# Kernel optimization log

Measured on AMD Instinct MI355X. Metric: run time of the kernel, lower is better.

The kernel has to match this reference:

```python
import jax, jax.numpy as jnp
import numpy as np

NEG = -1000000000.0

def setup_inputs() -> dict:
    key = jax.random.key(0)
    k1, k2, k3, k4 = jax.random.split(key, 4)
    B, T, D, V = 64, 512, 768, 20
    embeddings = jax.random.normal(k1, (B, T, D), dtype=jnp.float32)
    embeddings_mask = jax.random.randint(k2, (B, T), 0, 2, dtype=jnp.int32)
    value_mask = jax.random.randint(k3, (B, V), 0, 2, dtype=jnp.int32)
    value_weight = jax.random.normal(k4, (V, D), dtype=jnp.float32)
    return {"embeddings": embeddings, "embeddings_mask": embeddings_mask,
            "value_mask": value_mask, "value_weight": value_weight}

def reference(embeddings, embeddings_mask, value_mask, value_weight):
    # value attention: scores[b,t,v] = <emb[b,t], W[v]>  (torch does bcast-mul-sum)
    emb_mask = embeddings_mask.astype(jnp.float32)          # (B,T)
    scores = jnp.einsum('btd,vd->btv', embeddings, value_weight)
    scores = scores * emb_mask[:, :, None]                   # mask tokens
    value_scores = scores.sum(axis=1)                        # (B,V)
    value_scores = value_scores + (1.0 - value_mask.astype(jnp.float32)) * NEG
    value_probs = jax.nn.softmax(value_scores, axis=-1)      # (B,V)
    value_embedding = jnp.einsum('bv,vd->bd', value_probs, value_weight)
    # attention pooling over tokens using value_embedding as query
    pooling_scores = jnp.einsum('btd,bd->bt', embeddings, value_embedding)
    pooling_scores = pooling_scores + (1.0 - emb_mask) * NEG
    pooling_probs = jax.nn.softmax(pooling_scores, axis=-1)  # (B,T)
    pooled_embedding = jnp.einsum('btd,bt->bd', embeddings, pooling_probs)
    return (value_embedding, pooled_embedding, value_probs, pooling_probs)
```

## Files before the change

### kernel.cpp

```cpp
#include <hip/hip_runtime.h>
#include <math.h>

#define B 64
#define T 512
#define D 768
#define D4 192
#define V 20
#define NEG -1000000000.0f
#define TCH 32
#define NCH 16
#define NBLK (B * NCH)

__global__ __launch_bounds__(256) void k_sum_vdots(
    const float4* __restrict__ emb4, const int* __restrict__ emask,
    const float* __restrict__ W, float* __restrict__ pd) {
  const int bc = blockIdx.x, b = bc >> 4, c = bc & 15;
  const int tid = threadIdx.x, wave = tid >> 6, lane = tid & 63;
  __shared__ int sm[TCH];
  __shared__ int idx[TCH];
  __shared__ int scnt;
  __shared__ float4 lacc4[4][D4];
  __shared__ float msum[D];

  if (tid < TCH) sm[tid] = emask[b * T + c * TCH + tid];
  __syncthreads();
  if (tid == 0) {
    int n = 0;
    for (int t = 0; t < TCH; ++t)
      if (sm[t]) idx[n++] = t;
    scnt = n;
  }
  __syncthreads();
  const int cnt = scnt;
  const float4* eb = emb4 + ((size_t)b * T + (size_t)c * TCH) * D4;

  float4 s0 = {0.f, 0.f, 0.f, 0.f}, s1 = s0, s2 = s0;
  int i = wave;
  for (; i + 4 < cnt; i += 8) {
    const float4* ea = eb + (size_t)idx[i] * D4 + lane;
    const float4* ec = eb + (size_t)idx[i + 4] * D4 + lane;
    float4 a0 = ea[0], a1 = ea[64], a2 = ea[128];
    float4 b0 = ec[0], b1 = ec[64], b2 = ec[128];
    s0.x += a0.x + b0.x; s0.y += a0.y + b0.y;
    s0.z += a0.z + b0.z; s0.w += a0.w + b0.w;
    s1.x += a1.x + b1.x; s1.y += a1.y + b1.y;
    s1.z += a1.z + b1.z; s1.w += a1.w + b1.w;
    s2.x += a2.x + b2.x; s2.y += a2.y + b2.y;
    s2.z += a2.z + b2.z; s2.w += a2.w + b2.w;
  }
  if (i < cnt) {
    const float4* ea = eb + (size_t)idx[i] * D4 + lane;
    float4 a0 = ea[0], a1 = ea[64], a2 = ea[128];
    s0.x += a0.x; s0.y += a0.y; s0.z += a0.z; s0.w += a0.w;
    s1.x += a1.x; s1.y += a1.y; s1.z += a1.z; s1.w += a1.w;
    s2.x += a2.x; s2.y += a2.y; s2.z += a2.z; s2.w += a2.w;
  }
  lacc4[wave][lane] = s0;
  lacc4[wave][lane + 64] = s1;
  lacc4[wave][lane + 128] = s2;
  __syncthreads();
  if (tid < D4) {
    float4 a = lacc4[0][tid], x = lacc4[1][tid], y = lacc4[2][tid],
           z = lacc4[3][tid];
    float4 r;
    r.x = a.x + x.x + y.x + z.x;
    r.y = a.y + x.y + y.y + z.y;
    r.z = a.z + x.z + y.z + z.z;
    r.w = a.w + x.w + y.w + z.w;
    *(float4*)&msum[4 * tid] = r;
  }
  __syncthreads();
  for (int v = wave; v < V; v += 4) {
    float p = 0.f;
    const float* wv = W + (size_t)v * D;
    for (int j = 0; j < 12; ++j) {
      int d = lane + 64 * j;
      p += msum[d] * wv[d];
    }
    for (int off = 32; off; off >>= 1) p += __shfl_xor(p, off, 64);
    if (lane == 0) pd[bc * V + v] = p;
  }
}

__global__ __launch_bounds__(256) void k_fused_pool(
    const float4* __restrict__ emb4, const int* __restrict__ emask,
    const int* __restrict__ vmask, const float* __restrict__ W,
    const float* __restrict__ pd, float* __restrict__ vemb_out,
    float* __restrict__ vprobs_out, float* __restrict__ scores,
    float* __restrict__ pm, float* __restrict__ pl,
    float4* __restrict__ pacc4) {
  const int bc = blockIdx.x, b = bc >> 4, c = bc & 15;
  const int tid = threadIdx.x, wave = tid >> 6, lane = tid & 63;
  __shared__ int sm[TCH];
  __shared__ int idx[TCH];
  __shared__ int scnt;
  __shared__ float4 lacc4[4][D4];
  __shared__ float vemb[D];
  __shared__ float sc[V], pr[V];
  __shared__ float lm[4], ll[4], co4[4];

  if (tid < TCH) sm[tid] = emask[b * T + c * TCH + tid];
  __syncthreads();
  if (tid == 0) {
    int n = 0;
    for (int t = 0; t < TCH; ++t)
      if (sm[t]) idx[n++] = t;
    scnt = n;
  }

  if (tid < V) {
    float s = 0.f;
    for (int cc = 0; cc < NCH; ++cc) s += pd[(b * NCH + cc) * V + tid];
    sc[tid] = s + (vmask[b * V + tid] ? 0.f : NEG);
  }
  __syncthreads();
  if (tid == 0) {
    float m = sc[0];
    for (int v = 1; v < V; ++v) m = fmaxf(m, sc[v]);
    float ssum = 0.f;
    for (int v = 0; v < V; ++v) {
      float e = expf(sc[v] - m);
      pr[v] = e;
      ssum += e;
    }
    float inv = 1.f / ssum;
    for (int v = 0; v < V; ++v) {
      pr[v] *= inv;
      if (c == 0) vprobs_out[b * V + v] = pr[v];
    }
  }
  __syncthreads();
  for (int k = 0; k < 3; ++k) {
    int d = tid + 256 * k;
    float a = 0.f;
    for (int v = 0; v < V; ++v) a += pr[v] * W[(size_t)v * D + d];
    vemb[d] = a;
    if (c == 0) vemb_out[(size_t)b * D + d] = a;
  }
  __syncthreads();

  const int cnt = scnt;
  const float4* eb = emb4 + ((size_t)b * T + (size_t)c * TCH) * D4;
  const float4* vb = (const float4*)vemb;
  float4 ve0 = vb[lane], ve1 = vb[lane + 64], ve2 = vb[lane + 128];
  float* srow = scores + b * T + c * TCH;
  float m = NEG, l = 0.f;
  float4 a0 = {0.f, 0.f, 0.f, 0.f}, a1 = a0, a2 = a0;
  int i = wave;
  for (; i + 4 < cnt; i += 8) {
    int t0 = idx[i], t1 = idx[i + 4];
    const float4* ea = eb + (size_t)t0 * D4 + lane;
    const float4* ec = eb + (size_t)t1 * D4 + lane;
    float4 e0 = ea[0], e1 = ea[64], e2 = ea[128];
    float4 f0 = ec[0], f1 = ec[64], f2 = ec[128];
    float p0 = e0.x * ve0.x + e0.y * ve0.y + e0.z * ve0.z + e0.w * ve0.w +
               e1.x * ve1.x + e1.y * ve1.y + e1.z * ve1.z + e1.w * ve1.w +
               e2.x * ve2.x + e2.y * ve2.y + e2.z * ve2.z + e2.w * ve2.w;
    float p1 = f0.x * ve0.x + f0.y * ve0.y + f0.z * ve0.z + f0.w * ve0.w +
               f1.x * ve1.x + f1.y * ve1.y + f1.z * ve1.z + f1.w * ve1.w +
               f2.x * ve2.x + f2.y * ve2.y + f2.z * ve2.z + f2.w * ve2.w;
    for (int off = 32; off; off >>= 1) {
      p0 += __shfl_xor(p0, off, 64);
      p1 += __shfl_xor(p1, off, 64);
    }
    if (lane == 0) { srow[t0] = p0; srow[t1] = p1; }
    float mn = fmaxf(m, fmaxf(p0, p1));
    float scale = expf(m - mn);
    float w0 = expf(p0 - mn), w1 = expf(p1 - mn);
    l = l * scale + w0 + w1;
    a0.x = a0.x * scale + w0 * e0.x + w1 * f0.x;
    a0.y = a0.y * scale + w0 * e0.y + w1 * f0.y;
    a0.z = a0.z * scale + w0 * e0.z + w1 * f0.z;
    a0.w = a0.w * scale + w0 * e0.w + w1 * f0.w;
    a1.x = a1.x * scale + w0 * e1.x + w1 * f1.x;
    a1.y = a1.y * scale + w0 * e1.y + w1 * f1.y;
    a1.z = a1.z * scale + w0 * e1.z + w1 * f1.z;
    a1.w = a1.w * scale + w0 * e1.w + w1 * f1.w;
    a2.x = a2.x * scale + w0 * e2.x + w1 * f2.x;
    a2.y = a2.y * scale + w0 * e2.y + w1 * f2.y;
    a2.z = a2.z * scale + w0 * e2.z + w1 * f2.z;
    a2.w = a2.w * scale + w0 * e2.w + w1 * f2.w;
    m = mn;
  }
  if (i < cnt) {
    int t0 = idx[i];
    const float4* ea = eb + (size_t)t0 * D4 + lane;
    float4 e0 = ea[0], e1 = ea[64], e2 = ea[128];
    float p0 = e0.x * ve0.x + e0.y * ve0.y + e0.z * ve0.z + e0.w * ve0.w +
               e1.x * ve1.x + e1.y * ve1.y + e1.z * ve1.z + e1.w * ve1.w +
               e2.x * ve2.x + e2.y * ve2.y + e2.z * ve2.z + e2.w * ve2.w;
    for (int off = 32; off; off >>= 1) p0 += __shfl_xor(p0, off, 64);
    if (lane == 0) srow[t0] = p0;
    float mn = fmaxf(m, p0);
    float scale = expf(m - mn);
    float w0 = expf(p0 - mn);
    l = l * scale + w0;
    a0.x = a0.x * scale + w0 * e0.x; a0.y = a0.y * scale + w0 * e0.y;
    a0.z = a0.z * scale + w0 * e0.z; a0.w = a0.w * scale + w0 * e0.w;
    a1.x = a1.x * scale + w0 * e1.x; a1.y = a1.y * scale + w0 * e1.y;
    a1.z = a1.z * scale + w0 * e1.z; a1.w = a1.w * scale + w0 * e1.w;
    a2.x = a2.x * scale + w0 * e2.x; a2.y = a2.y * scale + w0 * e2.y;
    a2.z = a2.z * scale + w0 * e2.z; a2.w = a2.w * scale + w0 * e2.w;
    m = mn;
  }
  if (lane == 0) { lm[wave] = m; ll[wave] = l; }
  lacc4[wave][lane] = a0;
  lacc4[wave][lane + 64] = a1;
  lacc4[wave][lane + 128] = a2;
  __syncthreads();
  if (tid == 0) {
    float M = fmaxf(fmaxf(lm[0], lm[1]), fmaxf(lm[2], lm[3]));
    float L = 0.f;
    for (int w2 = 0; w2 < 4; ++w2) {
      float cw = expf(lm[w2] - M);
      co4[w2] = cw;
      L += ll[w2] * cw;
    }
    pm[bc] = M;
    pl[bc] = L;
  }
  __syncthreads();
  if (tid < D4) {
    float4 r = {0.f, 0.f, 0.f, 0.f};
    for (int w2 = 0; w2 < 4; ++w2) {
      float cw = co4[w2];
      float4 a = lacc4[w2][tid];
      r.x += cw * a.x; r.y += cw * a.y;
      r.z += cw * a.z; r.w += cw * a.w;
    }
    pacc4[(size_t)bc * D4 + tid] = r;
  }
}

__global__ __launch_bounds__(256) void k_finalize(
    const float* __restrict__ pm, const float* __restrict__ pl,
    const float4* __restrict__ pacc4, const float* __restrict__ scores,
    const int* __restrict__ emask, float* __restrict__ pooled,
    float* __restrict__ pprobs) {
  const int b = blockIdx.x, tid = threadIdx.x;
  __shared__ float co[NCH];
  __shared__ float sM, sinvL;
  if (tid == 0) {
    float M = NEG;
    for (int cc = 0; cc < NCH; ++cc) M = fmaxf(M, pm[b * NCH + cc]);
    float L = 0.f;
    for (int cc = 0; cc < NCH; ++cc)
      L += pl[b * NCH + cc] * expf(pm[b * NCH + cc] - M);
    float invL = 1.f / L;
    for (int cc = 0; cc < NCH; ++cc)
      co[cc] = expf(pm[b * NCH + cc] - M) * invL;
    sM = M;
    sinvL = invL;
  }
  __syncthreads();
  if (tid < D4) {
    float4 r = {0.f, 0.f, 0.f, 0.f};
    for (int cc = 0; cc < NCH; ++cc) {
      float cw = co[cc];
      float4 a = pacc4[(size_t)(b * NCH + cc) * D4 + tid];
      r.x += cw * a.x; r.y += cw * a.y;
      r.z += cw * a.z; r.w += cw * a.w;
    }
    ((float4*)pooled)[(size_t)b * D4 + tid] = r;
  }
  float M = sM, invL = sinvL;
  for (int k = 0; k < 2; ++k) {
    int t = tid + 256 * k;
    pprobs[b * T + t] =
        emask[b * T + t] ? expf(scores[b * T + t] - M) * invL : 0.f;
  }
}

extern "C" void kernel_launch(void* const* d_in, const int* in_sizes, int n_in,
                              void* d_out, int out_size, void* d_ws,
                              size_t ws_size, hipStream_t stream) {
  const float4* emb4 = (const float4*)d_in[0];
  const int* emask = (const int*)d_in[1];
  const int* vmask = (const int*)d_in[2];
  const float* W = (const float*)d_in[3];

  float* out = (float*)d_out;
  float* vemb_out = out;
  float* pooled_out = out + B * D;
  float* vprobs_out = out + 2 * B * D;
  float* pprobs_out = out + 2 * B * D + B * V;

  float* ws = (float*)d_ws;
  float* pacc = ws;
  float* scores = pacc + NBLK * D;
  float* pm = scores + B * T;
  float* pl = pm + NBLK;
  float* pd = pl + NBLK;

  k_sum_vdots<<<dim3(NBLK), dim3(256), 0, stream>>>(emb4, emask, W, pd);
  k_fused_pool<<<dim3(NBLK), dim3(256), 0, stream>>>(
      emb4, emask, vmask, W, pd, vemb_out, vprobs_out, scores, pm, pl,
      (float4*)pacc);
  k_finalize<<<dim3(B), dim3(256), 0, stream>>>(pm, pl, (const float4*)pacc,
                                                scores, emask, pooled_out,
                                                pprobs_out);
}
```

Before: 165.6 us.

## Unroll token loops to four rows, ballot-compact mask, use fast exp

The token-gather loops in both streaming kernels now load four masked rows per iteration instead of two, putting more independent global loads in flight per wave. The serial single-thread mask compaction is replaced by a wave ballot plus popcount prefix. expf is swapped for __expf throughout, and launch bounds now request occupancy of 4 blocks. These add register pressure and slightly lower exp accuracy, and the tail loops now step by four rows.

```diff
diff --git a/kernel.cpp b/kernel.cpp
--- a/kernel.cpp
+++ b/kernel.cpp
@@ -11,46 +11,61 @@
 #define NCH 16
 #define NBLK (B * NCH)
 
-__global__ __launch_bounds__(256) void k_sum_vdots(
+__device__ __forceinline__ void compact_idx(const int* sm, int* idx,
+                                            int* scnt, int tid) {
+  if (tid < 64) {
+    unsigned long long bal = __ballot(tid < TCH && sm[tid]);
+    if (tid < TCH && sm[tid]) {
+      int pos = __popcll(bal & ((1ull << tid) - 1ull));
+      idx[pos] = tid;
+    }
+    if (tid == 0) *scnt = (int)__popcll(bal);
+  }
+}
+
+__global__ __launch_bounds__(256, 4) void k_sum_vdots(
     const float4* __restrict__ emb4, const int* __restrict__ emask,
     const float* __restrict__ W, float* __restrict__ pd) {
   const int bc = blockIdx.x, b = bc >> 4, c = bc & 15;
   const int tid = threadIdx.x, wave = tid >> 6, lane = tid & 63;
-  __shared__ int sm[TCH];
-  __shared__ int idx[TCH];
-  __shared__ int scnt;
+  __shared__ int sm[TCH], idx[TCH], scnt;
   __shared__ float4 lacc4[4][D4];
   __shared__ float msum[D];
 
   if (tid < TCH) sm[tid] = emask[b * T + c * TCH + tid];
   __syncthreads();
-  if (tid == 0) {
-    int n = 0;
-    for (int t = 0; t < TCH; ++t)
-      if (sm[t]) idx[n++] = t;
-    scnt = n;
-  }
+  compact_idx(sm, idx, &scnt, tid);
   __syncthreads();
   const int cnt = scnt;
   const float4* eb = emb4 + ((size_t)b * T + (size_t)c * TCH) * D4;
 
   float4 s0 = {0.f, 0.f, 0.f, 0.f}, s1 = s0, s2 = s0;
   int i = wave;
-  for (; i + 4 < cnt; i += 8) {
-    const float4* ea = eb + (size_t)idx[i] * D4 + lane;
-    const float4* ec = eb + (size_t)idx[i + 4] * D4 + lane;
-    float4 a0 = ea[0], a1 = ea[64], a2 = ea[128];
-    float4 b0 = ec[0], b1 = ec[64], b2 = ec[128];
-    s0.x += a0.x + b0.x; s0.y += a0.y + b0.y;
-    s0.z += a0.z + b0.z; s0.w += a0.w + b0.w;
-    s1.x += a1.x + b1.x; s1.y += a1.y + b1.y;
-    s1.z += a1.z + b1.z; s1.w += a1.w + b1.w;
-    s2.x += a2.x + b2.x; s2.y += a2.y + b2.y;
-    s2.z += a2.z + b2.z; s2.w += a2.w + b2.w;
-  }
-  if (i < cnt) {
-    const float4* ea = eb + (size_t)idx[i] * D4 + lane;
-    float4 a0 = ea[0], a1 = ea[64], a2 = ea[128];
+  for (; i + 12 < cnt; i += 16) {
+    const float4* p0 = eb + (size_t)idx[i] * D4 + lane;
+    const float4* p1 = eb + (size_t)idx[i + 4] * D4 + lane;
+    const float4* p2 = eb + (size_t)idx[i + 8] * D4 + lane;
+    const float4* p3 = eb + (size_t)idx[i + 12] * D4 + lane;
+    float4 a0 = p0[0], a1 = p0[64], a2 = p0[128];
+    float4 b0 = p1[0], b1 = p1[64], b2 = p1[128];
+    float4 c0 = p2[0], c1 = p2[64], c2 = p2[128];
+    float4 d0 = p3[0], d1 = p3[64], d2 = p3[128];
+    s0.x += (a0.x + b0.x) + (c0.x + d0.x);
+    s0.y += (a0.y + b0.y) + (c0.y + d0.y);
+    s0.z += (a0.z + b0.z) + (c0.z + d0.z);
+    s0.w += (a0.w + b0.w) + (c0.w + d0.w);
+    s1.x += (a1.x + b1.x) + (c1.x + d1.x);
+    s1.y += (a1.y + b1.y) + (c1.y + d1.y);
+    s1.z += (a1.z + b1.z) + (c1.z + d1.z);
+    s1.w += (a1.w + b1.w) + (c1.w + d1.w);
+    s2.x += (a2.x + b2.x) + (c2.x + d2.x);
+    s2.y += (a2.y + b2.y) + (c2.y + d2.y);
+    s2.z += (a2.z + b2.z) + (c2.z + d2.z);
+    s2.w += (a2.w + b2.w) + (c2.w + d2.w);
+  }
+  for (; i < cnt; i += 4) {
+    const float4* p0 = eb + (size_t)idx[i] * D4 + lane;
+    float4 a0 = p0[0], a1 = p0[64], a2 = p0[128];
     s0.x += a0.x; s0.y += a0.y; s0.z += a0.z; s0.w += a0.w;
     s1.x += a1.x; s1.y += a1.y; s1.z += a1.z; s1.w += a1.w;
     s2.x += a2.x; s2.y += a2.y; s2.z += a2.z; s2.w += a2.w;
@@ -82,7 +97,7 @@
   }
 }
 
-__global__ __launch_bounds__(256) void k_fused_pool(
+__global__ __launch_bounds__(256, 4) void k_fused_pool(
     const float4* __restrict__ emb4, const int* __restrict__ emask,
     const int* __restrict__ vmask, const float* __restrict__ W,
     const float* __restrict__ pd, float* __restrict__ vemb_out,
@@ -91,9 +106,7 @@
     float4* __restrict__ pacc4) {
   const int bc = blockIdx.x, b = bc >> 4, c = bc & 15;
   const int tid = threadIdx.x, wave = tid >> 6, lane = tid & 63;
-  __shared__ int sm[TCH];
-  __shared__ int idx[TCH];
-  __shared__ int scnt;
+  __shared__ int sm[TCH], idx[TCH], scnt;
   __shared__ float4 lacc4[4][D4];
   __shared__ float vemb[D];
   __shared__ float sc[V], pr[V];
@@ -101,12 +114,7 @@
 
   if (tid < TCH) sm[tid] = emask[b * T + c * TCH + tid];
   __syncthreads();
-  if (tid == 0) {
-    int n = 0;
-    for (int t = 0; t < TCH; ++t)
-      if (sm[t]) idx[n++] = t;
-    scnt = n;
-  }
+  compact_idx(sm, idx, &scnt, tid);
 
   if (tid < V) {
     float s = 0.f;
@@ -119,7 +127,7 @@
     for (int v = 1; v < V; ++v) m = fmaxf(m, sc[v]);
     float ssum = 0.f;
     for (int v = 0; v < V; ++v) {
-      float e = expf(sc[v] - m);
+      float e = __expf(sc[v] - m);
       pr[v] = e;
       ssum += e;
     }
@@ -147,60 +155,75 @@
   float m = NEG, l = 0.f;
   float4 a0 = {0.f, 0.f, 0.f, 0.f}, a1 = a0, a2 = a0;
   int i = wave;
-  for (; i + 4 < cnt; i += 8) {
-    int t0 = idx[i], t1 = idx[i + 4];
-    const float4* ea = eb + (size_t)t0 * D4 + lane;
-    const float4* ec = eb + (size_t)t1 * D4 + lane;
-    float4 e0 = ea[0], e1 = ea[64], e2 = ea[128];
-    float4 f0 = ec[0], f1 = ec[64], f2 = ec[128];
+  for (; i + 12 < cnt; i += 16) {
+    int t0 = idx[i], t1 = idx[i + 4], t2 = idx[i + 8], t3 = idx[i + 12];
+    const float4* q0 = eb + (size_t)t0 * D4 + lane;
+    const float4* q1 = eb + (size_t)t1 * D4 + lane;
+    const float4* q2 = eb + (size_t)t2 * D4 + lane;
+    const float4* q3 = eb + (size_t)t3 * D4 + lane;
+    float4 e0 = q0[0], e1 = q0[64], e2 = q0[128];
+    float4 f0 = q1[0], f1 = q1[64], f2 = q1[128];
+    float4 g0 = q2[0], g1 = q2[64], g2 = q2[128];
+    float4 h0 = q3[0], h1 = q3[64], h2 = q3[128];
     float p0 = e0.x * ve0.x + e0.y * ve0.y + e0.z * ve0.z + e0.w * ve0.w +
                e1.x * ve1.x + e1.y * ve1.y + e1.z * ve1.z + e1.w * ve1.w +
                e2.x * ve2.x + e2.y * ve2.y + e2.z * ve2.z + e2.w * ve2.w;
     float p1 = f0.x * ve0.x + f0.y * ve0.y + f0.z * ve0.z + f0.w * ve0.w +
                f1.x * ve1.x + f1.y * ve1.y + f1.z * ve1.z + f1.w * ve1.w +
                f2.x * ve2.x + f2.y * ve2.y + f2.z * ve2.z + f2.w * ve2.w;
+    float p2 = g0.x * ve0.x + g0.y * ve0.y + g0.z * ve0.z + g0.w * ve0.w +
+               g1.x * ve1.x + g1.y * ve1.y + g1.z * ve1.z + g1.w * ve1.w +
+               g2.x * ve2.x + g2.y * ve2.y + g2.z * ve2.z + g2.w * ve2.w;
+    float p3 = h0.x * ve0.x + h0.y * ve0.y + h0.z * ve0.z + h0.w * ve0.w +
+               h1.x * ve1.x + h1.y * ve1.y + h1.z * ve1.z + h1.w * ve1.w +
+               h2.x * ve2.x + h2.y * ve2.y + h2.z * ve2.z + h2.w * ve2.w;
     for (int off = 32; off; off >>= 1) {
       p0 += __shfl_xor(p0, off, 64);
       p1 += __shfl_xor(p1, off, 64);
-    }
-    if (lane == 0) { srow[t0] = p0; srow[t1] = p1; }
-    float mn = fmaxf(m, fmaxf(p0, p1));
-    float scale = expf(m - mn);
-    float w0 = expf(p0 - mn), w1 = expf(p1 - mn);
-    l = l * scale + w0 + w1;
-    a0.x = a0.x * scale + w0 * e0.x + w1 * f0.x;
-    a0.y = a0.y * scale + w0 * e0.y + w1 * f0.y;
-    a0.z = a0.z * scale + w0 * e0.z + w1 * f0.z;
-    a0.w = a0.w * scale + w0 * e0.w + w1 * f0.w;
-    a1.x = a1.x * scale + w0 * e1.x + w1 * f1.x;
-    a1.y = a1.y * scale + w0 * e1.y + w1 * f1.y;
-    a1.z = a1.z * scale + w0 * e1.z + w1 * f1.z;
-    a1.w = a1.w * scale + w0 * e1.w + w1 * f1.w;
-    a2.x = a2.x * scale + w0 * e2.x + w1 * f2.x;
-    a2.y = a2.y * scale + w0 * e2.y + w1 * f2.y;
-    a2.z = a2.z * scale + w0 * e2.z + w1 * f2.z;
-    a2.w = a2.w * scale + w0 * e2.w + w1 * f2.w;
+      p2 += __shfl_xor(p2, off, 64);
+      p3 += __shfl_xor(p3, off, 64);
+    }
+    if (lane == 0) {
+      srow[t0] = p0; srow[t1] = p1; srow[t2] = p2; srow[t3] = p3;
+    }
+    float mn = fmaxf(fmaxf(m, fmaxf(p0, p1)), fmaxf(p2, p3));
+    float scale = __expf(m - mn);
+    float w0 = __expf(p0 - mn), w1 = __expf(p1 - mn);
+    float w2 = __expf(p2 - mn), w3 = __expf(p3 - mn);
+    l = l * scale + (w0 + w1) + (w2 + w3);
+    a0.x = a0.x * scale + w0 * e0.x + w1 * f0.x + w2 * g0.x + w3 * h0.x;
+    a0.y = a0.y * scale + w0 * e0.y + w1 * f0.y + w2 * g0.y + w3 * h0.y;
+    a0.z = a0.z * scale + w0 * e0.z + w1 * f0.z + w2 * g0.z + w3 * h0.z;
+    a0.w = a0.w * scale + w0 * e0.w + w1 * f0.w + w2 * g0.w + w3 * h0.w;
+    a1.x = a1.x * scale + w0 * e1.x + w1 * f1.x + w2 * g1.x + w3 * h1.x;
+    a1.y = a1.y * scale + w0 * e1.y + w1 * f1.y + w2 * g1.y + w3 * h1.y;
+    a1.z = a1.z * scale + w0 * e1.z + w1 * f1.z + w2 * g1.z + w3 * h1.z;
+    a1.w = a1.w * scale + w0 * e1.w + w1 * f1.w + w2 * g1.w + w3 * h1.w;
+    a2.x = a2.x * scale + w0 * e2.x + w1 * f2.x + w2 * g2.x + w3 * h2.x;
+    a2.y = a2.y * scale + w0 * e2.y + w1 * f2.y + w2 * g2.y + w3 * h2.y;
+    a2.z = a2.z * scale + w0 * e2.z + w1 * f2.z + w2 * g2.z + w3 * h2.z;
+    a2.w = a2.w * scale + w0 * e2.w + w1 * f2.w + w2 * g2.w + w3 * h2.w;
     m = mn;
   }
-  if (i < cnt) {
+  for (; i < cnt; i += 4) {
     int t0 = idx[i];
-    const float4* ea = eb + (size_t)t0 * D4 + lane;
-    float4 e0 = ea[0], e1 = ea[64], e2 = ea[128];
+    const float4* q0 = eb + (size_t)t0 * D4 + lane;
+    float4 e0 = q0[0], e1 = q0[64], e2 = q0[128];
     float p0 = e0.x * ve0.x + e0.y * ve0.y + e0.z * ve0.z + e0.w * ve0.w +
                e1.x * ve1.x + e1.y * ve1.y + e1.z * ve1.z + e1.w * ve1.w +
                e2.x * ve2.x + e2.y * ve2.y + e2.z * ve2.z + e2.w * ve2.w;
     for (int off = 32; off; off >>= 1) p0 += __shfl_xor(p0, off, 64);
     if (lane == 0) srow[t0] = p0;
     float mn = fmaxf(m, p0);
-    float scale = expf(m - mn);
-    float w0 = expf(p0 - mn);
+    float scale = __expf(m - mn);
+    float w0 = __expf(p0 - mn);
     l = l * scale + w0;
     a0.x = a0.x * scale + w0 * e0.x; a0.y = a0.y * scale + w0 * e0.y;
     a0.z = a0.z * scale + w0 * e0.z; a0.w = a0.w * scale + w0 * e0.w;
     a1.x = a1.x * scale + w0 * e1.x; a1.y = a1.y * scale + w0 * e1.y;
     a1.z = a1.z * scale + w0 * e1.z; a1.w = a1.w * scale + w0 * e1.w;
     a2.x = a2.x * scale + w0 * e2.x; a2.y = a2.y * scale + w0 * e2.y;
-    a2.z = a2.z * scale + w0 * e2.z; a2.w = a2.w * scale + w0 * e2.w;
+    a2.w = a2.w * scale + w0 * e2.w; a2.z = a2.z * scale + w0 * e2.z;
     m = mn;
   }
   if (lane == 0) { lm[wave] = m; ll[wave] = l; }
@@ -212,7 +235,7 @@
     float M = fmaxf(fmaxf(lm[0], lm[1]), fmaxf(lm[2], lm[3]));
     float L = 0.f;
     for (int w2 = 0; w2 < 4; ++w2) {
-      float cw = expf(lm[w2] - M);
+      float cw = __expf(lm[w2] - M);
       co4[w2] = cw;
       L += ll[w2] * cw;
     }
@@ -245,10 +268,10 @@
     for (int cc = 0; cc < NCH; ++cc) M = fmaxf(M, pm[b * NCH + cc]);
     float L = 0.f;
     for (int cc = 0; cc < NCH; ++cc)
-      L += pl[b * NCH + cc] * expf(pm[b * NCH + cc] - M);
+      L += pl[b * NCH + cc] * __expf(pm[b * NCH + cc] - M);
     float invL = 1.f / L;
     for (int cc = 0; cc < NCH; ++cc)
-      co[cc] = expf(pm[b * NCH + cc] - M) * invL;
+      co[cc] = __expf(pm[b * NCH + cc] - M) * invL;
     sM = M;
     sinvL = invL;
   }
@@ -267,7 +290,7 @@
   for (int k = 0; k < 2; ++k) {
     int t = tid + 256 * k;
     pprobs[b * T + t] =
-        emask[b * T + t] ? expf(scores[b * T + t] - M) * invL : 0.f;
+        emask[b * T + t] ? __expf(scores[b * T + t] - M) * invL : 0.f;
   }
 }
 
```

New measurement: 161.7 us. 2.3% less time.
